# Optimization experiments

Hardware: AMD Instinct MI355X
Metric: run time of the kernel (lower is better)

The kernel has to match this reference:

```python
import jax, jax.numpy as jnp
import numpy as np

B, N, INP, OUP = 16, 1024, 512, 512
HEADS, DIM_HEAD = 8, 64
INNER = HEADS * DIM_HEAD


def setup_inputs() -> dict:
    key = jax.random.key(0)
    ks = jax.random.split(key, 9)
    return {
        "query": jax.random.normal(ks[0], (B, N, INP), jnp.float32),
        "key": jax.random.normal(ks[1], (B, N, INP), jnp.float32),
        "value": jax.random.normal(ks[2], (B, N, INP), jnp.float32),
        "Wq": jax.random.normal(ks[3], (INP, INNER), jnp.float32) * 0.02,
        "Wk": jax.random.normal(ks[4], (INP, INNER), jnp.float32) * 0.02,
        "Wv": jax.random.normal(ks[5], (INP, INNER), jnp.float32) * 0.02,
        "Wo": jax.random.normal(ks[6], (INNER, OUP), jnp.float32) * 0.02,
        "bo": jax.random.normal(ks[7], (OUP,), jnp.float32) * 0.02,
        "bias_table": jax.random.normal(ks[8], (2 * N - 1, HEADS), jnp.float32) * 0.02,
    }


def reference(query, key, value, Wq, Wk, Wv, Wo, bo, bias_table):
    scale = DIM_HEAD ** -0.5
    split = lambda t: t.reshape(B, N, HEADS, DIM_HEAD).transpose(0, 2, 1, 3)  # b h n d
    q = split(query @ Wq)
    k = split(key @ Wk)
    v = split(value @ Wv)
    dots = jnp.einsum("bhnd,bhmd->bhnm", q, k) * scale
    # relative position index: (i - j) + (N - 1), shape [N, N]
    coords = jnp.arange(N)
    rel_idx = coords[:, None] - coords[None, :] + (N - 1)
    rel_bias = bias_table[rel_idx]            # [N, N, H]
    rel_bias = rel_bias.transpose(2, 0, 1)[None]  # [1, H, N, N]
    attn = jax.nn.softmax(dots + rel_bias, axis=-1)
    out = jnp.einsum("bhnm,bhmd->bhnd", attn, v)
    out = out.transpose(0, 2, 1, 3).reshape(B, N, INNER)
    return out @ Wo + bo
```

## Files before the change

### kernel.cpp

```cpp
#include <hip/hip_runtime.h>
#include <hip/hip_bf16.h>
#include <stdint.h>

#define BB 16
#define SEQ 1024
#define CHN 512
#define NH 8
#define DH 64

typedef short short8 __attribute__((ext_vector_type(8)));
typedef short short4v __attribute__((ext_vector_type(4)));
typedef float f32x4 __attribute__((ext_vector_type(4)));

typedef const __attribute__((address_space(1))) unsigned int* gptr_t;
typedef __attribute__((address_space(3))) unsigned int* lptr_t;

__device__ __forceinline__ void async16(const void* g, void* l) {
    __builtin_amdgcn_global_load_lds((gptr_t)g, (lptr_t)l, 16, 0, 0);
}

__device__ __forceinline__ unsigned short f2bf(float f) {
    unsigned int u = __float_as_uint(f);
    u += 0x7FFF + ((u >> 16) & 1);
    return (unsigned short)(u >> 16);
}

__global__ __launch_bounds__(256) void k_cvt3(const float* __restrict__ a, const float* __restrict__ b,
                                              const float* __restrict__ c,
                                              unsigned short* __restrict__ oa, unsigned short* __restrict__ ob,
                                              unsigned short* __restrict__ oc, int n4) {
    int i = blockIdx.x * 256 + threadIdx.x;
    if (i >= n4) return;
    const float* in = (blockIdx.y == 0) ? a : (blockIdx.y == 1) ? b : c;
    unsigned short* out = (blockIdx.y == 0) ? oa : (blockIdx.y == 1) ? ob : oc;
    float4 v = ((const float4*)in)[i];
    ushort4 o;
    o.x = f2bf(v.x); o.y = f2bf(v.y); o.z = f2bf(v.z); o.w = f2bf(v.w);
    ((ushort4*)out)[i] = o;
}

__global__ __launch_bounds__(256) void k_cvtw4(const float* __restrict__ W0, const float* __restrict__ W1,
                                               const float* __restrict__ W2, const float* __restrict__ W3,
                                               unsigned short* __restrict__ T0, unsigned short* __restrict__ T1,
                                               unsigned short* __restrict__ T2, unsigned short* __restrict__ T3) {
    __shared__ float t[32][33];
    int z = blockIdx.z;
    const float* W = (z == 0) ? W0 : (z == 1) ? W1 : (z == 2) ? W2 : W3;
    unsigned short* Wt = (z == 0) ? T0 : (z == 1) ? T1 : (z == 2) ? T2 : T3;
    int n0 = blockIdx.x * 32, k0 = blockIdx.y * 32;
    int tx = threadIdx.x & 31, ty = threadIdx.x >> 5;
    for (int r = ty; r < 32; r += 8) t[r][tx] = W[(k0 + r) * CHN + n0 + tx];
    __syncthreads();
    for (int r = ty; r < 32; r += 8) Wt[(n0 + r) * CHN + k0 + tx] = f2bf(t[tx][r]);
}

__device__ __forceinline__ void gemm_tile64(const unsigned short* __restrict__ A,
                                            const unsigned short* __restrict__ Bt,
                                            int Kdim, int m0, int n0,
                                            f32x4 acc[4][4],
                                            unsigned short* As, unsigned short* Bs) {
    const int tid = threadIdx.x;
    const int lane = tid & 63, wid = tid >> 6;
    const int g = lane >> 4, l16 = lane & 15;
    const int wm = wid >> 1, wn = wid & 1;
    for (int i = 0; i < 4; i++)
        for (int j = 0; j < 4; j++) acc[i][j] = (f32x4){0.f, 0.f, 0.f, 0.f};
    for (int k0 = 0; k0 < Kdim; k0 += 64) {
        for (int c = 0; c < 4; ++c) {
            int seg = c * 256 + tid;
            int row = seg >> 3, ch = seg & 7;
            const unsigned short* ga = A + (size_t)(m0 + row) * Kdim + k0 + ch * 8;
            const unsigned short* gb = Bt + (size_t)(n0 + row) * Kdim + k0 + ch * 8;
            int base = (c * 256 + wid * 64) * 8;
            async16(ga, As + base);
            async16(gb, Bs + base);
        }
        __syncthreads();
        for (int kk = 0; kk < 64; kk += 32) {
            short8 af[4], bfr[4];
            for (int mi = 0; mi < 4; mi++)
                af[mi] = *(const short8*)(As + (wm * 64 + mi * 16 + l16) * 64 + kk + g * 8);
            for (int ni = 0; ni < 4; ni++)
                bfr[ni] = *(const short8*)(Bs + (wn * 64 + ni * 16 + l16) * 64 + kk + g * 8);
            for (int mi = 0; mi < 4; mi++)
                for (int ni = 0; ni < 4; ni++)
                    acc[mi][ni] = __builtin_amdgcn_mfma_f32_16x16x32_bf16(af[mi], bfr[ni], acc[mi][ni], 0, 0, 0);
        }
        __syncthreads();
    }
}

__global__ __launch_bounds__(256) void k_gemm_qkv(
    const unsigned short* __restrict__ Xq, const unsigned short* __restrict__ Xk,
    const unsigned short* __restrict__ Xv,
    const unsigned short* __restrict__ Wtq, const unsigned short* __restrict__ Wtk,
    const unsigned short* __restrict__ Wtv,
    unsigned short* __restrict__ Qp, unsigned short* __restrict__ Kp,
    unsigned short* __restrict__ Vtp) {
    __shared__ unsigned short As[128 * 64], Bs[128 * 64];
    int z = blockIdx.z;
    const unsigned short* A = (z == 0) ? Xq : (z == 1) ? Xk : Xv;
    const unsigned short* Bt = (z == 0) ? Wtq : (z == 1) ? Wtk : Wtv;
    int m0 = blockIdx.y * 128, n0 = blockIdx.x * 128;
    f32x4 acc[4][4];
    gemm_tile64(A, Bt, CHN, m0, n0, acc, As, Bs);

    const int tid = threadIdx.x, lane = tid & 63, wid = tid >> 6;
    const int g = lane >> 4, l16 = lane & 15;
    const int wm = wid >> 1, wn = wid & 1;
    const float QSC = 0.125f * 1.4426950408889634f;
    if (z < 2) {
        unsigned short* dst = (z == 0) ? Qp : Kp;
        const float sc = (z == 0) ? QSC : 1.0f;
        for (int mi = 0; mi < 4; mi++)
            for (int ni = 0; ni < 4; ni++) {
                int col = n0 + wn * 64 + ni * 16 + l16;
                int h = col >> 6, d = col & 63;
                for (int r = 0; r < 4; r++) {
                    int m = m0 + wm * 64 + mi * 16 + g * 4 + r;
                    int b = m >> 10, i = m & 1023;
                    dst[(((size_t)b * NH + h) * SEQ + i) * DH + d] = f2bf(acc[mi][ni][r] * sc);
                }
            }
    } else {
        for (int mi = 0; mi < 4; mi++)
            for (int ni = 0; ni < 4; ni++) {
                int col = n0 + wn * 64 + ni * 16 + l16;
                int h = col >> 6, d = col & 63;
                int m = m0 + wm * 64 + mi * 16 + g * 4;
                int b = m >> 10, i = m & 1023;
                ushort4 pk;
                pk.x = f2bf(acc[mi][ni][0]); pk.y = f2bf(acc[mi][ni][1]);
                pk.z = f2bf(acc[mi][ni][2]); pk.w = f2bf(acc[mi][ni][3]);
                *(ushort4*)&Vtp[(((size_t)b * NH + h) * DH + d) * SEQ + i] = pk;
            }
    }
}

__global__ __launch_bounds__(512, 6) void k_attn(const unsigned short* __restrict__ Qp,
                                                 const unsigned short* __restrict__ Kp,
                                                 const unsigned short* __restrict__ Vtp,
                                                 const float* __restrict__ bias_table,
                                                 unsigned short* __restrict__ AO) {
    __shared__ unsigned short K_lds[64 * 72];
    __shared__ unsigned short V_lds[64 * 72];
    __shared__ uint2 biasq[1152];
    const int bh = blockIdx.y;
    const int h = bh & (NH - 1);
    const int i0blk = blockIdx.x * 128;
    const int tid = threadIdx.x, lane = tid & 63, w = tid >> 6;
    const int g = lane >> 4, l16 = lane & 15;
    const unsigned short* Qb = Qp + (size_t)bh * SEQ * DH;
    const unsigned short* Kb = Kp + (size_t)bh * SEQ * DH;
    const unsigned short* Vb = Vtp + (size_t)bh * DH * SEQ;

    const float LOG2E = 1.4426950408889634f;
    for (int t = tid; t < 1148; t += 512) {
        const float* bp = bias_table + (size_t)(t + i0blk) * NH + h;
        unsigned int b0 = f2bf(bp[0 * NH] * LOG2E), b1 = f2bf(bp[1 * NH] * LOG2E);
        unsigned int b2 = f2bf(bp[2 * NH] * LOG2E), b3 = f2bf(bp[3 * NH] * LOG2E);
        uint2 q; q.x = (b1 << 16) | b0; q.y = (b3 << 16) | b2;
        biasq[t] = q;
    }

    const int iw = i0blk + w * 16;
    short8 qf[2];
    for (int f = 0; f < 2; f++)
        qf[f] = *(const short8*)(Qb + (iw + l16) * DH + f * 32 + g * 8);

    float lsum = 0.f;
    f32x4 acc[4];
    for (int db = 0; db < 4; db++) acc[db] = (f32x4){0.f, 0.f, 0.f, 0.f};

    const int r0 = tid >> 3, c0 = tid & 7;
    int4 kr = *(const int4*)(Kb + (size_t)r0 * DH + c0 * 8);
    int4 vr = *(const int4*)(Vb + (size_t)r0 * SEQ + c0 * 8);

    for (int j0 = 0; j0 < SEQ; j0 += 64) {
        *(int4*)(&K_lds[r0 * 72 + c0 * 8]) = kr;
        *(int4*)(&V_lds[r0 * 72 + c0 * 8]) = vr;
        __syncthreads();

        if (j0 + 64 < SEQ) {
            const int jn = j0 + 64;
            kr = *(const int4*)(Kb + (size_t)(jn + r0) * DH + c0 * 8);
            vr = *(const int4*)(Vb + (size_t)r0 * SEQ + jn + c0 * 8);
        }

        const int bb0 = (w * 16 + l16 + 1023) - j0 - g * 4;
        for (int jb = 0; jb < 4; jb++) {
            short8 kf0 = *(const short8*)(&K_lds[(jb * 16 + l16) * 72 + g * 8]);
            short8 kf1 = *(const short8*)(&K_lds[(jb * 16 + l16) * 72 + 32 + g * 8]);
            const int bb = bb0 - jb * 16;
            const uint2 bq = biasq[bb - 3];
            f32x4 s4 = {__uint_as_float(bq.y & 0xffff0000u),
                        __uint_as_float(bq.y << 16),
                        __uint_as_float(bq.x & 0xffff0000u),
                        __uint_as_float(bq.x << 16)};
            s4 = __builtin_amdgcn_mfma_f32_16x16x32_bf16(kf0, qf[0], s4, 0, 0, 0);
            s4 = __builtin_amdgcn_mfma_f32_16x16x32_bf16(kf1, qf[1], s4, 0, 0, 0);
            float p0 = __builtin_amdgcn_exp2f(s4[0]);
            float p1 = __builtin_amdgcn_exp2f(s4[1]);
            float p2 = __builtin_amdgcn_exp2f(s4[2]);
            float p3 = __builtin_amdgcn_exp2f(s4[3]);
            lsum += (p0 + p1) + (p2 + p3);
            uint2 pkd;
            pkd.x = (unsigned int)f2bf(p0) | ((unsigned int)f2bf(p1) << 16);
            pkd.y = (unsigned int)f2bf(p2) | ((unsigned int)f2bf(p3) << 16);
            short4v pk = __builtin_bit_cast(short4v, pkd);
            for (int db = 0; db < 4; db++) {
                short4v vf = *(const short4v*)(&V_lds[(db * 16 + l16) * 72 + jb * 16 + g * 4]);
                acc[db] = __builtin_amdgcn_mfma_f32_16x16x16bf16_1k(vf, pk, acc[db], 0, 0, 0);
            }
        }
        __syncthreads();
    }

    float v = lsum;
    v += __shfl_xor(v, 16, 64);
    v += __shfl_xor(v, 32, 64);
    const float inv = 1.0f / v;

    const int b = bh >> 3;
    const int i = iw + l16;
    for (int db = 0; db < 4; db++) {
        ushort4 o;
        o.x = f2bf(acc[db][0] * inv);
        o.y = f2bf(acc[db][1] * inv);
        o.z = f2bf(acc[db][2] * inv);
        o.w = f2bf(acc[db][3] * inv);
        *(ushort4*)&AO[((size_t)b * SEQ + i) * CHN + h * DH + db * 16 + g * 4] = o;
    }
}

__global__ __launch_bounds__(256) void k_gemm_out(const unsigned short* __restrict__ AOb,
                                                  const unsigned short* __restrict__ Wto,
                                                  const float* __restrict__ bo,
                                                  float* __restrict__ out) {
    __shared__ unsigned short As[128 * 64], Bs[128 * 64];
    int m0 = blockIdx.y * 128, n0 = blockIdx.x * 128;
    f32x4 acc[4][4];
    gemm_tile64(AOb, Wto, CHN, m0, n0, acc, As, Bs);
    const int tid = threadIdx.x, lane = tid & 63, wid = tid >> 6;
    const int g = lane >> 4, l16 = lane & 15;
    const int wm = wid >> 1, wn = wid & 1;
    for (int ni = 0; ni < 4; ni++) {
        int col = n0 + wn * 64 + ni * 16 + l16;
        float bias = bo[col];
        for (int mi = 0; mi < 4; mi++)
            for (int r = 0; r < 4; r++) {
                int m = m0 + wm * 64 + mi * 16 + g * 4 + r;
                out[(size_t)m * CHN + col] = acc[mi][ni][r] + bias;
            }
    }
}

extern "C" void kernel_launch(void* const* d_in, const int* in_sizes, int n_in,
                              void* d_out, int out_size, void* d_ws, size_t ws_size,
                              hipStream_t stream) {
    const float* q_f = (const float*)d_in[0];
    const float* k_f = (const float*)d_in[1];
    const float* v_f = (const float*)d_in[2];
    const float* Wq_f = (const float*)d_in[3];
    const float* Wk_f = (const float*)d_in[4];
    const float* Wv_f = (const float*)d_in[5];
    const float* Wo_f = (const float*)d_in[6];
    const float* bo_f = (const float*)d_in[7];
    const float* bt_f = (const float*)d_in[8];

    char* ws = (char*)d_ws;
    const size_t S_X = (size_t)BB * SEQ * CHN * 2;
    const size_t S_W = (size_t)CHN * CHN * 2;

    unsigned short* Xq = (unsigned short*)(ws);
    unsigned short* Xk = (unsigned short*)(ws + S_X);
    unsigned short* Xv = (unsigned short*)(ws + 2 * S_X);
    unsigned short* Wtq = (unsigned short*)(ws + 3 * S_X);
    unsigned short* Wtk = (unsigned short*)(ws + 3 * S_X + S_W);
    unsigned short* Wtv = (unsigned short*)(ws + 3 * S_X + 2 * S_W);
    unsigned short* Wto = (unsigned short*)(ws + 3 * S_X + 3 * S_W);
    unsigned short* Qp = (unsigned short*)(ws + 3 * S_X + 4 * S_W);
    unsigned short* Kp = (unsigned short*)(ws + 4 * S_X + 4 * S_W);
    unsigned short* Vtp = (unsigned short*)(ws + 5 * S_X + 4 * S_W);
    unsigned short* AO = Xq;

    const int n4 = BB * SEQ * CHN / 4;
    k_cvt3<<<dim3(n4 / 256, 3), 256, 0, stream>>>(q_f, k_f, v_f, Xq, Xk, Xv, n4);
    k_cvtw4<<<dim3(16, 16, 4), 256, 0, stream>>>(Wq_f, Wk_f, Wv_f, Wo_f, Wtq, Wtk, Wtv, Wto);

    k_gemm_qkv<<<dim3(CHN / 128, BB * SEQ / 128, 3), 256, 0, stream>>>(
        Xq, Xk, Xv, Wtq, Wtk, Wtv, Qp, Kp, Vtp);

    k_attn<<<dim3(SEQ / 128, BB * NH), 512, 0, stream>>>(Qp, Kp, Vtp, bt_f, AO);

    k_gemm_out<<<dim3(CHN / 128, BB * SEQ / 128), 256, 0, stream>>>(
        AO, Wto, bo_f, (float*)d_out);
}
```

Baseline: 169.9 us.

## Process two 16-row query fragments per wave in attention to reuse K/V fragments

Each wave in the attention kernel now handles 32 query rows as two MFMA fragments instead of 16. Each block covers 256 query rows, so the grid along the sequence is halved. Every K and V fragment read from LDS, and every K/V tile staged per block, now feeds twice the MFMA work, which cuts LDS and global traffic per output. In exchange the kernel uses more registers (launch bounds lowered to 4 blocks), has a larger bias buffer, and launches half as many blocks (512 total), which could hurt occupancy and CU fill.

```diff
diff --git a/kernel.cpp b/kernel.cpp
--- a/kernel.cpp
+++ b/kernel.cpp
@@ -137,17 +137,17 @@
     }
 }
 
-__global__ __launch_bounds__(512, 6) void k_attn(const unsigned short* __restrict__ Qp,
+__global__ __launch_bounds__(512, 4) void k_attn(const unsigned short* __restrict__ Qp,
                                                  const unsigned short* __restrict__ Kp,
                                                  const unsigned short* __restrict__ Vtp,
                                                  const float* __restrict__ bias_table,
                                                  unsigned short* __restrict__ AO) {
     __shared__ unsigned short K_lds[64 * 72];
     __shared__ unsigned short V_lds[64 * 72];
-    __shared__ uint2 biasq[1152];
+    __shared__ uint2 biasq[1280];
     const int bh = blockIdx.y;
     const int h = bh & (NH - 1);
-    const int i0blk = blockIdx.x * 128;
+    const int i0blk = blockIdx.x * 256;
     const int tid = threadIdx.x, lane = tid & 63, w = tid >> 6;
     const int g = lane >> 4, l16 = lane & 15;
     const unsigned short* Qb = Qp + (size_t)bh * SEQ * DH;
@@ -155,7 +155,7 @@
     const unsigned short* Vb = Vtp + (size_t)bh * DH * SEQ;
 
     const float LOG2E = 1.4426950408889634f;
-    for (int t = tid; t < 1148; t += 512) {
+    for (int t = tid; t < 1276; t += 512) {
         const float* bp = bias_table + (size_t)(t + i0blk) * NH + h;
         unsigned int b0 = f2bf(bp[0 * NH] * LOG2E), b1 = f2bf(bp[1 * NH] * LOG2E);
         unsigned int b2 = f2bf(bp[2 * NH] * LOG2E), b3 = f2bf(bp[3 * NH] * LOG2E);
@@ -163,14 +163,16 @@
         biasq[t] = q;
     }
 
-    const int iw = i0blk + w * 16;
-    short8 qf[2];
-    for (int f = 0; f < 2; f++)
-        qf[f] = *(const short8*)(Qb + (iw + l16) * DH + f * 32 + g * 8);
-
-    float lsum = 0.f;
-    f32x4 acc[4];
-    for (int db = 0; db < 4; db++) acc[db] = (f32x4){0.f, 0.f, 0.f, 0.f};
+    const int iw = i0blk + w * 32;
+    short8 qf[2][2];
+    for (int mf = 0; mf < 2; mf++)
+        for (int f = 0; f < 2; f++)
+            qf[mf][f] = *(const short8*)(Qb + (iw + mf * 16 + l16) * DH + f * 32 + g * 8);
+
+    float lsum0 = 0.f, lsum1 = 0.f;
+    f32x4 acc[2][4];
+    for (int mf = 0; mf < 2; mf++)
+        for (int db = 0; db < 4; db++) acc[mf][db] = (f32x4){0.f, 0.f, 0.f, 0.f};
 
     const int r0 = tid >> 3, c0 = tid & 7;
     int4 kr = *(const int4*)(Kb + (size_t)r0 * DH + c0 * 8);
@@ -187,49 +189,71 @@
             vr = *(const int4*)(Vb + (size_t)r0 * SEQ + jn + c0 * 8);
         }
 
-        const int bb0 = (w * 16 + l16 + 1023) - j0 - g * 4;
+        const int bbB = (w * 32 + l16 + 1023) - j0 - g * 4;
         for (int jb = 0; jb < 4; jb++) {
             short8 kf0 = *(const short8*)(&K_lds[(jb * 16 + l16) * 72 + g * 8]);
             short8 kf1 = *(const short8*)(&K_lds[(jb * 16 + l16) * 72 + 32 + g * 8]);
-            const int bb = bb0 - jb * 16;
-            const uint2 bq = biasq[bb - 3];
-            f32x4 s4 = {__uint_as_float(bq.y & 0xffff0000u),
-                        __uint_as_float(bq.y << 16),
-                        __uint_as_float(bq.x & 0xffff0000u),
-                        __uint_as_float(bq.x << 16)};
-            s4 = __builtin_amdgcn_mfma_f32_16x16x32_bf16(kf0, qf[0], s4, 0, 0, 0);
-            s4 = __builtin_amdgcn_mfma_f32_16x16x32_bf16(kf1, qf[1], s4, 0, 0, 0);
-            float p0 = __builtin_amdgcn_exp2f(s4[0]);
-            float p1 = __builtin_amdgcn_exp2f(s4[1]);
-            float p2 = __builtin_amdgcn_exp2f(s4[2]);
-            float p3 = __builtin_amdgcn_exp2f(s4[3]);
-            lsum += (p0 + p1) + (p2 + p3);
-            uint2 pkd;
-            pkd.x = (unsigned int)f2bf(p0) | ((unsigned int)f2bf(p1) << 16);
-            pkd.y = (unsigned int)f2bf(p2) | ((unsigned int)f2bf(p3) << 16);
-            short4v pk = __builtin_bit_cast(short4v, pkd);
+            const int bb0 = bbB - jb * 16;
+            const uint2 bq0 = biasq[bb0 - 3];
+            const uint2 bq1 = biasq[bb0 + 13];
+            f32x4 s0 = {__uint_as_float(bq0.y & 0xffff0000u),
+                        __uint_as_float(bq0.y << 16),
+                        __uint_as_float(bq0.x & 0xffff0000u),
+                        __uint_as_float(bq0.x << 16)};
+            f32x4 s1 = {__uint_as_float(bq1.y & 0xffff0000u),
+                        __uint_as_float(bq1.y << 16),
+                        __uint_as_float(bq1.x & 0xffff0000u),
+                        __uint_as_float(bq1.x << 16)};
+            s0 = __builtin_amdgcn_mfma_f32_16x16x32_bf16(kf0, qf[0][0], s0, 0, 0, 0);
+            s0 = __builtin_amdgcn_mfma_f32_16x16x32_bf16(kf1, qf[0][1], s0, 0, 0, 0);
+            s1 = __builtin_amdgcn_mfma_f32_16x16x32_bf16(kf0, qf[1][0], s1, 0, 0, 0);
+            s1 = __builtin_amdgcn_mfma_f32_16x16x32_bf16(kf1, qf[1][1], s1, 0, 0, 0);
+            float p00 = __builtin_amdgcn_exp2f(s0[0]);
+            float p01 = __builtin_amdgcn_exp2f(s0[1]);
+            float p02 = __builtin_amdgcn_exp2f(s0[2]);
+            float p03 = __builtin_amdgcn_exp2f(s0[3]);
+            float p10 = __builtin_amdgcn_exp2f(s1[0]);
+            float p11 = __builtin_amdgcn_exp2f(s1[1]);
+            float p12 = __builtin_amdgcn_exp2f(s1[2]);
+            float p13 = __builtin_amdgcn_exp2f(s1[3]);
+            lsum0 += (p00 + p01) + (p02 + p03);
+            lsum1 += (p10 + p11) + (p12 + p13);
+            uint2 pd0, pd1;
+            pd0.x = (unsigned int)f2bf(p00) | ((unsigned int)f2bf(p01) << 16);
+            pd0.y = (unsigned int)f2bf(p02) | ((unsigned int)f2bf(p03) << 16);
+            pd1.x = (unsigned int)f2bf(p10) | ((unsigned int)f2bf(p11) << 16);
+            pd1.y = (unsigned int)f2bf(p12) | ((unsigned int)f2bf(p13) << 16);
+            short4v pk0 = __builtin_bit_cast(short4v, pd0);
+            short4v pk1 = __builtin_bit_cast(short4v, pd1);
             for (int db = 0; db < 4; db++) {
                 short4v vf = *(const short4v*)(&V_lds[(db * 16 + l16) * 72 + jb * 16 + g * 4]);
-                acc[db] = __builtin_amdgcn_mfma_f32_16x16x16bf16_1k(vf, pk, acc[db], 0, 0, 0);
+                acc[0][db] = __builtin_amdgcn_mfma_f32_16x16x16bf16_1k(vf, pk0, acc[0][db], 0, 0, 0);
+                acc[1][db] = __builtin_amdgcn_mfma_f32_16x16x16bf16_1k(vf, pk1, acc[1][db], 0, 0, 0);
             }
         }
         __syncthreads();
     }
 
-    float v = lsum;
-    v += __shfl_xor(v, 16, 64);
-    v += __shfl_xor(v, 32, 64);
-    const float inv = 1.0f / v;
+    float v0 = lsum0, v1 = lsum1;
+    v0 += __shfl_xor(v0, 16, 64);
+    v0 += __shfl_xor(v0, 32, 64);
+    v1 += __shfl_xor(v1, 16, 64);
+    v1 += __shfl_xor(v1, 32, 64);
+    const float inv0 = 1.0f / v0;
+    const float inv1 = 1.0f / v1;
 
     const int b = bh >> 3;
-    const int i = iw + l16;
-    for (int db = 0; db < 4; db++) {
-        ushort4 o;
-        o.x = f2bf(acc[db][0] * inv);
-        o.y = f2bf(acc[db][1] * inv);
-        o.z = f2bf(acc[db][2] * inv);
-        o.w = f2bf(acc[db][3] * inv);
-        *(ushort4*)&AO[((size_t)b * SEQ + i) * CHN + h * DH + db * 16 + g * 4] = o;
+    for (int mf = 0; mf < 2; mf++) {
+        const float inv = mf ? inv1 : inv0;
+        const int i = iw + mf * 16 + l16;
+        for (int db = 0; db < 4; db++) {
+            ushort4 o;
+            o.x = f2bf(acc[mf][db][0] * inv);
+            o.y = f2bf(acc[mf][db][1] * inv);
+            o.z = f2bf(acc[mf][db][2] * inv);
+            o.w = f2bf(acc[mf][db][3] * inv);
+            *(ushort4*)&AO[((size_t)b * SEQ + i) * CHN + h * DH + db * 16 + g * 4] = o;
+        }
     }
 }
 
@@ -291,7 +315,7 @@
     k_gemm_qkv<<<dim3(CHN / 128, BB * SEQ / 128, 3), 256, 0, stream>>>(
         Xq, Xk, Xv, Wtq, Wtk, Wtv, Qp, Kp, Vtp);
 
-    k_attn<<<dim3(SEQ / 128, BB * NH), 512, 0, stream>>>(Qp, Kp, Vtp, bt_f, AO);
+    k_attn<<<dim3(SEQ / 256, BB * NH), 512, 0, stream>>>(Qp, Kp, Vtp, bt_f, AO);
 
     k_gemm_out<<<dim3(CHN / 128, BB * SEQ / 128), 256, 0, stream>>>(
         AO, Wto, bo_f, (float*)d_out);
```

Result: faster. 155.7 us, median of 2 (-8.4%).
